# Performance work log

Measured on AMD Instinct MI355X. Metric: run time of the kernel, lower is better.

Reference implementation:

```python
import jax, jax.numpy as jnp
import numpy as np

B, R, A, S, F, N = 2, 1, 16, 14, 1024, 512  # batch, num_rx, num_rx_ant, ofdm_symbols, fft_size, num_effective_sc
D = S * N  # flattened time-frequency dim that C acts on


def setup_inputs() -> dict:
    key = jax.random.key(0)
    k0, k1, k2, k3 = jax.random.split(key, 4)
    scale = 1.0 / np.sqrt(D).astype(np.float32)
    x_re = jax.random.normal(k0, (B, R, A, S, F), jnp.float32)
    x_im = jax.random.normal(k1, (B, R, A, S, F), jnp.float32)
    C_re = jax.random.normal(k2, (D, D), jnp.float32) * scale
    C_im = jax.random.normal(k3, (D, D), jnp.float32) * scale
    # unique, sorted effective-subcarrier indices (as in an OFDM ResourceGrid)
    sc_ind = jnp.asarray(np.sort(np.random.default_rng(0).choice(F, N, replace=False)), jnp.int32)
    return {"x_re": x_re, "x_im": x_im, "C_re": C_re, "C_im": C_im, "sc_ind": sc_ind}


def reference(x_re, x_im, C_re, C_im, sc_ind):
    x = jax.lax.complex(x_re, x_im)            # [B,R,A,S,F] complex64
    C = jax.lax.complex(C_re, C_im)            # [D,D]
    y = jnp.take(x, sc_ind, axis=-1)           # gather effective subcarriers -> [B,R,A,S,N]
    b, r, a, s, n = y.shape
    yf = y.reshape(b, r, a, s * n)             # flatten_last_dims(y, 2)
    # multiply_from_right with adjoint: yf @ C^H
    yf = jnp.einsum('brad,ed->brae', yf, jnp.conj(C))
    y = yf.reshape(b, r, a, s, n)
    # scatter back into full fft_size grid (unique indices -> set == scatter_nd on zeros)
    out = jnp.zeros((b, r, a, s, F), y.dtype).at[..., sc_ind].set(y)
    return jnp.stack([out.real, out.imag])     # [2,B,R,A,S,F] (real, imag)
```

## Files before the change

kernel.cpp:

```cpp
#include <hip/hip_runtime.h>
#include <hip/hip_bf16.h>

#define B_ 2
#define R_ 1
#define A_ 16
#define S_ 14
#define F_ 1024
#define N_ 512
#define D_ (S_*N_)
#define M_ (B_*R_*A_)
#define KK_ (2*D_)
#define BE 64
#define ETILES (D_/BE)

typedef __attribute__((ext_vector_type(8))) short bf16x8;
typedef __attribute__((ext_vector_type(4))) float f32x4;

static __device__ inline short f2bf(float f) {
    __hip_bfloat16 h = __float2bfloat16(f);
    return *reinterpret_cast<short*>(&h);
}
static __device__ inline float bf2f(short s) {
    unsigned int u = ((unsigned int)(unsigned short)s) << 16;
    return __uint_as_float(u);
}

#define LDSP(p) ((__attribute__((address_space(3))) void*)(p))
#define GLBP(p) ((const __attribute__((address_space(1))) void*)(p))

__global__ void prep_kernel(const float* __restrict__ xr, const float* __restrict__ xi,
                            const int* __restrict__ sc, short* __restrict__ Ap) {
    int idx = blockIdx.x * blockDim.x + threadIdx.x;
    if (idx >= 64 * KK_) return;
    int k = idx % KK_;
    int r = idx / KK_;
    int m = r & 31;
    int half = (k >= D_) ? 1 : 0;
    int d = half ? (k - D_) : k;
    int s = d >> 9;
    int n = d & 511;
    int f = sc[n];
    const float* base = (r < 32) ? (half ? xi : xr) : (half ? xr : xi);
    float v = base[(m * S_ + s) * F_ + f];
    if (r >= 32 && half) v = -v;
    Ap[((size_t)(k >> 3) * 64 + r) * 8 + (k & 7)] = f2bf(v);
}

__global__ void zero_kernel(float4* __restrict__ out, int n4) {
    int i = blockIdx.x * blockDim.x + threadIdx.x;
    if (i < n4) out[i] = make_float4(0.f, 0.f, 0.f, 0.f);
}

template<int KSPLIT, int PARTIALS>
__global__ __launch_bounds__(256) void gemm_kernel(
    const short* __restrict__ Ap,
    const float* __restrict__ Cre, const float* __restrict__ Cim,
    const int* __restrict__ sc,
    void* __restrict__ outp)
{
    constexpr int KBLK = KK_ / KSPLIT;
    constexpr int NCH  = KBLK / 32;
    __shared__ float Bl[3][64 * 32];
    __shared__ short Al[3][64 * 32];

    const int etile = blockIdx.x;
    const int ks    = blockIdx.y;
    const int tid   = threadIdx.x;
    const int wave  = tid >> 6;
    const int lane  = tid & 63;
    const int l16   = lane & 15;
    const int kg    = lane >> 4;

    const float* Cp = (ks < KSPLIT / 2) ? Cre : Cim;
    const int kc = (ks % (KSPLIT / 2)) * KBLK;
    const int ka = ks * KBLK;

    const float* bsrc[2];
    #pragma unroll
    for (int q = 0; q < 2; ++q) {
        int U = q * 256 + tid;
        int row = U >> 3;
        int u = (U & 7) ^ (row & 7);
        bsrc[q] = Cp + (size_t)(etile * BE + row) * D_ + kc + u * 4;
    }
    const short* asrc = Ap + ((size_t)(ka >> 3) * 64) * 8 + tid * 8;

#define STAGE(c) do { \
        int bf_ = (c) % 3; \
        __builtin_amdgcn_global_load_lds(GLBP(bsrc[0] + (size_t)(c) * 32), \
                                         LDSP(&Bl[bf_][(0 * 256 + tid) * 4]), 16, 0, 0); \
        __builtin_amdgcn_global_load_lds(GLBP(bsrc[1] + (size_t)(c) * 32), \
                                         LDSP(&Bl[bf_][(1 * 256 + tid) * 4]), 16, 0, 0); \
        __builtin_amdgcn_global_load_lds(GLBP(asrc + (size_t)(c) * 2048), \
                                         LDSP(&Al[bf_][tid * 8]), 16, 0, 0); \
    } while (0)

    STAGE(0);
    STAGE(1);

    f32x4 acc0 = {0.f,0.f,0.f,0.f}, acc1 = {0.f,0.f,0.f,0.f};
    f32x4 acc2 = {0.f,0.f,0.f,0.f}, acc3 = {0.f,0.f,0.f,0.f};

    const int row  = wave * 16 + l16;
    const int swz  = row & 7;
    const int boff = row * 32;
    const int u0 = ((kg * 2 + 0) ^ swz) * 4;
    const int u1 = ((kg * 2 + 1) ^ swz) * 4;

    for (int c = 0; c < NCH; ++c) {
        if (c < NCH - 1) asm volatile("s_waitcnt vmcnt(3)" ::: "memory");
        else             asm volatile("s_waitcnt vmcnt(0)" ::: "memory");
        __builtin_amdgcn_sched_barrier(0);
        __builtin_amdgcn_s_barrier();

        const int buf = c % 3;
        f32x4 b0 = *reinterpret_cast<const f32x4*>(&Bl[buf][boff + u0]);
        f32x4 b1 = *reinterpret_cast<const f32x4*>(&Bl[buf][boff + u1]);
        bf16x8 a0 = *reinterpret_cast<const bf16x8*>(&Al[buf][(kg * 64 + 0 * 16 + l16) * 8]);
        bf16x8 a1 = *reinterpret_cast<const bf16x8*>(&Al[buf][(kg * 64 + 1 * 16 + l16) * 8]);
        bf16x8 a2 = *reinterpret_cast<const bf16x8*>(&Al[buf][(kg * 64 + 2 * 16 + l16) * 8]);
        bf16x8 a3 = *reinterpret_cast<const bf16x8*>(&Al[buf][(kg * 64 + 3 * 16 + l16) * 8]);
        asm volatile("s_waitcnt lgkmcnt(0)" ::: "memory");
        __builtin_amdgcn_sched_barrier(0);
        __builtin_amdgcn_s_barrier();

        if (c + 2 < NCH) STAGE(c + 2);

        bf16x8 bfv;
        bfv[0] = f2bf(b0.x); bfv[1] = f2bf(b0.y); bfv[2] = f2bf(b0.z); bfv[3] = f2bf(b0.w);
        bfv[4] = f2bf(b1.x); bfv[5] = f2bf(b1.y); bfv[6] = f2bf(b1.z); bfv[7] = f2bf(b1.w);
        acc0 = __builtin_amdgcn_mfma_f32_16x16x32_bf16(a0, bfv, acc0, 0, 0, 0);
        acc1 = __builtin_amdgcn_mfma_f32_16x16x32_bf16(a1, bfv, acc1, 0, 0, 0);
        acc2 = __builtin_amdgcn_mfma_f32_16x16x32_bf16(a2, bfv, acc2, 0, 0, 0);
        acc3 = __builtin_amdgcn_mfma_f32_16x16x32_bf16(a3, bfv, acc3, 0, 0, 0);
    }
#undef STAGE

    const int e_lane = etile * BE + row;
    if (PARTIALS) {
        short* part = (short*)outp + (size_t)ks * (64 * D_);
        #pragma unroll
        for (int mt = 0; mt < 4; ++mt) {
            f32x4 a = (mt == 0) ? acc0 : (mt == 1) ? acc1 : (mt == 2) ? acc2 : acc3;
            int rbase = mt * 16 + kg * 4;
            #pragma unroll
            for (int r = 0; r < 4; ++r)
                part[(size_t)(rbase + r) * D_ + e_lane] = f2bf(a[r]);
        }
    } else {
        float* out = (float*)outp;
        int s = e_lane >> 9, n = e_lane & 511;
        int f = sc[n];
        #pragma unroll
        for (int mt = 0; mt < 4; ++mt) {
            f32x4 a = (mt == 0) ? acc0 : (mt == 1) ? acc1 : (mt == 2) ? acc2 : acc3;
            int rbase = mt * 16 + kg * 4;
            #pragma unroll
            for (int r = 0; r < 4; ++r) {
                int rr = rbase + r;
                int pp = rr >> 5, m = rr & 31;
                atomicAdd(&out[((pp * M_ + m) * S_ + s) * F_ + f], a[r]);
            }
        }
    }
}

template<int KSPLIT>
__global__ void reduce_kernel(const short* __restrict__ part, const int* __restrict__ sc,
                              float* __restrict__ out) {
    int t = blockIdx.x * blockDim.x + threadIdx.x;
    if (t >= 64 * D_ / 8) return;
    int base = t * 8;
    int e0 = base % D_;
    int r  = base / D_;
    float v[8] = {0.f,0.f,0.f,0.f,0.f,0.f,0.f,0.f};
    #pragma unroll
    for (int ksp = 0; ksp < KSPLIT; ++ksp) {
        bf16x8 x = *reinterpret_cast<const bf16x8*>(&part[(size_t)ksp * (64 * D_) + base]);
        #pragma unroll
        for (int j = 0; j < 8; ++j) v[j] += bf2f(x[j]);
    }
    int pp = r >> 5, m = r & 31, s = e0 >> 9, n0 = e0 & 511;
    float* ob = &out[((pp * M_ + m) * S_ + s) * F_];
    #pragma unroll
    for (int j = 0; j < 8; ++j) ob[sc[n0 + j]] = v[j];
}

extern "C" void kernel_launch(void* const* d_in, const int* in_sizes, int n_in,
                              void* d_out, int out_size, void* d_ws, size_t ws_size,
                              hipStream_t stream) {
    const float* xr  = (const float*)d_in[0];
    const float* xi  = (const float*)d_in[1];
    const float* Cre = (const float*)d_in[2];
    const float* Cim = (const float*)d_in[3];
    const int*   sc  = (const int*)d_in[4];
    float* out = (float*)d_out;

    short* Ap = (short*)d_ws;
    const size_t partOff = 2u * 1024u * 1024u;
    const size_t need28  = partOff + 28ull * 64 * D_ * 2;
    const size_t need16  = partOff + 16ull * 64 * D_ * 2;

    prep_kernel<<<dim3((64 * KK_ + 255) / 256), 256, 0, stream>>>(xr, xi, sc, Ap);
    zero_kernel<<<dim3((917504 / 4 + 255) / 256), 256, 0, stream>>>((float4*)out, 917504 / 4);

    const int rthreads = 64 * D_ / 8;
    if (ws_size >= need28) {
        short* part = (short*)((char*)d_ws + partOff);
        gemm_kernel<28, 1><<<dim3(ETILES, 28), 256, 0, stream>>>(Ap, Cre, Cim, sc, part);
        reduce_kernel<28><<<dim3((rthreads + 255) / 256), 256, 0, stream>>>(part, sc, out);
    } else if (ws_size >= need16) {
        short* part = (short*)((char*)d_ws + partOff);
        gemm_kernel<16, 1><<<dim3(ETILES, 16), 256, 0, stream>>>(Ap, Cre, Cim, sc, part);
        reduce_kernel<16><<<dim3((rthreads + 255) / 256), 256, 0, stream>>>(part, sc, out);
    } else {
        gemm_kernel<16, 0><<<dim3(ETILES, 16), 256, 0, stream>>>(Ap, Cre, Cim, sc, out);
    }
}
```

Measured before the change: 107.7 us.

## Make each wave load its own tiles and drop block barriers in split-K GEMM

```diff
diff --git a/kernel.cpp b/kernel.cpp
--- a/kernel.cpp
+++ b/kernel.cpp
@@ -51,8 +51,109 @@
     if (i < n4) out[i] = make_float4(0.f, 0.f, 0.f, 0.f);
 }
 
+__global__ __launch_bounds__(256) void gemm_wasync(
+    const short* __restrict__ Ap,
+    const float* __restrict__ Cre, const float* __restrict__ Cim,
+    short* __restrict__ part_all)
+{
+    constexpr int KSPLIT = 28;
+    constexpr int KBLK = KK_ / KSPLIT;
+    constexpr int NCH  = KBLK / 32;
+    __shared__ float Bl[4][3][16 * 32];
+    __shared__ short Al[4][3][64 * 32];
+
+    const int etile = blockIdx.x;
+    const int ks    = blockIdx.y;
+    const int tid   = threadIdx.x;
+    const int wave  = tid >> 6;
+    const int lane  = tid & 63;
+    const int l16   = lane & 15;
+    const int kg    = lane >> 4;
+
+    const float* Cp = (ks < 14) ? Cre : Cim;
+    const int kc = (ks % 14) * KBLK;
+    const int ka = ks * KBLK;
+
+    const int U0 = lane, U1 = 64 + lane;
+    const float* bsrc0 = Cp + (size_t)(etile * 64 + wave * 16 + (U0 >> 3)) * D_
+                            + kc + ((U0 & 7) ^ ((U0 >> 3) & 7)) * 4;
+    const float* bsrc1 = Cp + (size_t)(etile * 64 + wave * 16 + (U1 >> 3)) * D_
+                            + kc + ((U1 & 7) ^ ((U1 >> 3) & 7)) * 4;
+    const short* asrc = Ap + (size_t)(ka >> 3) * 512 + lane * 8;
+
+#define WAITV(n) asm volatile("s_waitcnt vmcnt(" #n ")" ::: "memory")
+#define STAGE(cc) do { \
+        int bb = (cc) % 3; \
+        __builtin_amdgcn_global_load_lds(GLBP(bsrc0 + (size_t)(cc) * 32), \
+                                         LDSP(&Bl[wave][bb][lane * 4]), 16, 0, 0); \
+        __builtin_amdgcn_global_load_lds(GLBP(bsrc1 + (size_t)(cc) * 32), \
+                                         LDSP(&Bl[wave][bb][(64 + lane) * 4]), 16, 0, 0); \
+        __builtin_amdgcn_global_load_lds(GLBP(asrc + (size_t)(cc) * 2048 + 0 * 512), \
+                                         LDSP(&Al[wave][bb][lane * 8]), 16, 0, 0); \
+        __builtin_amdgcn_global_load_lds(GLBP(asrc + (size_t)(cc) * 2048 + 1 * 512), \
+                                         LDSP(&Al[wave][bb][(64 + lane) * 8]), 16, 0, 0); \
+        __builtin_amdgcn_global_load_lds(GLBP(asrc + (size_t)(cc) * 2048 + 2 * 512), \
+                                         LDSP(&Al[wave][bb][(128 + lane) * 8]), 16, 0, 0); \
+        __builtin_amdgcn_global_load_lds(GLBP(asrc + (size_t)(cc) * 2048 + 3 * 512), \
+                                         LDSP(&Al[wave][bb][(192 + lane) * 8]), 16, 0, 0); \
+    } while (0)
+
+    STAGE(0);
+    STAGE(1);
+    STAGE(2);
+
+    f32x4 acc0 = {0.f,0.f,0.f,0.f}, acc1 = {0.f,0.f,0.f,0.f};
+    f32x4 acc2 = {0.f,0.f,0.f,0.f}, acc3 = {0.f,0.f,0.f,0.f};
+
+    const int swz  = l16 & 7;
+    const int boff = l16 * 32;
+    const int u0x = ((kg * 2 + 0) ^ swz) * 4;
+    const int u1x = ((kg * 2 + 1) ^ swz) * 4;
+
+    for (int c = 0; c < NCH; ++c) {
+        if (c <= NCH - 3)      { WAITV(12); }
+        else if (c == NCH - 2) { WAITV(6); }
+        else                   { WAITV(0); }
+        __builtin_amdgcn_sched_barrier(0);
+
+        const int buf = c % 3;
+        f32x4 b0 = *reinterpret_cast<const f32x4*>(&Bl[wave][buf][boff + u0x]);
+        f32x4 b1 = *reinterpret_cast<const f32x4*>(&Bl[wave][buf][boff + u1x]);
+        bf16x8 a0 = *reinterpret_cast<const bf16x8*>(&Al[wave][buf][(kg * 64 + 0 * 16 + l16) * 8]);
+        bf16x8 a1 = *reinterpret_cast<const bf16x8*>(&Al[wave][buf][(kg * 64 + 1 * 16 + l16) * 8]);
+        bf16x8 a2 = *reinterpret_cast<const bf16x8*>(&Al[wave][buf][(kg * 64 + 2 * 16 + l16) * 8]);
+        bf16x8 a3 = *reinterpret_cast<const bf16x8*>(&Al[wave][buf][(kg * 64 + 3 * 16 + l16) * 8]);
+        asm volatile("s_waitcnt lgkmcnt(0)" ::: "memory");
+        __builtin_amdgcn_sched_barrier(0);
+
+        if (c + 3 < NCH) STAGE(c + 3);
+        __builtin_amdgcn_sched_barrier(0);
+
+        bf16x8 bfv;
+        bfv[0] = f2bf(b0.x); bfv[1] = f2bf(b0.y); bfv[2] = f2bf(b0.z); bfv[3] = f2bf(b0.w);
+        bfv[4] = f2bf(b1.x); bfv[5] = f2bf(b1.y); bfv[6] = f2bf(b1.z); bfv[7] = f2bf(b1.w);
+        acc0 = __builtin_amdgcn_mfma_f32_16x16x32_bf16(a0, bfv, acc0, 0, 0, 0);
+        acc1 = __builtin_amdgcn_mfma_f32_16x16x32_bf16(a1, bfv, acc1, 0, 0, 0);
+        acc2 = __builtin_amdgcn_mfma_f32_16x16x32_bf16(a2, bfv, acc2, 0, 0, 0);
+        acc3 = __builtin_amdgcn_mfma_f32_16x16x32_bf16(a3, bfv, acc3, 0, 0, 0);
+    }
+#undef STAGE
+#undef WAITV
+
+    const int e_lane = etile * 64 + wave * 16 + l16;
+    short* part = part_all + (size_t)ks * (64 * D_);
+    #pragma unroll
+    for (int mt = 0; mt < 4; ++mt) {
+        f32x4 a = (mt == 0) ? acc0 : (mt == 1) ? acc1 : (mt == 2) ? acc2 : acc3;
+        int rbase = mt * 16 + kg * 4;
+        #pragma unroll
+        for (int r = 0; r < 4; ++r)
+            part[(size_t)(rbase + r) * D_ + e_lane] = f2bf(a[r]);
+    }
+}
+
 template<int KSPLIT, int PARTIALS>
-__global__ __launch_bounds__(256) void gemm_kernel(
+__global__ __launch_bounds__(256) void gemm_sync(
     const short* __restrict__ Ap,
     const float* __restrict__ Cre, const float* __restrict__ Cim,
     const int* __restrict__ sc,
@@ -60,8 +161,8 @@
 {
     constexpr int KBLK = KK_ / KSPLIT;
     constexpr int NCH  = KBLK / 32;
-    __shared__ float Bl[3][64 * 32];
-    __shared__ short Al[3][64 * 32];
+    __shared__ float Bls[3][64 * 32];
+    __shared__ short Als[3][64 * 32];
 
     const int etile = blockIdx.x;
     const int ks    = blockIdx.y;
@@ -85,18 +186,18 @@
     }
     const short* asrc = Ap + ((size_t)(ka >> 3) * 64) * 8 + tid * 8;
 
-#define STAGE(c) do { \
+#define STG(c) do { \
         int bf_ = (c) % 3; \
         __builtin_amdgcn_global_load_lds(GLBP(bsrc[0] + (size_t)(c) * 32), \
-                                         LDSP(&Bl[bf_][(0 * 256 + tid) * 4]), 16, 0, 0); \
+                                         LDSP(&Bls[bf_][(0 * 256 + tid) * 4]), 16, 0, 0); \
         __builtin_amdgcn_global_load_lds(GLBP(bsrc[1] + (size_t)(c) * 32), \
-                                         LDSP(&Bl[bf_][(1 * 256 + tid) * 4]), 16, 0, 0); \
+                                         LDSP(&Bls[bf_][(1 * 256 + tid) * 4]), 16, 0, 0); \
         __builtin_amdgcn_global_load_lds(GLBP(asrc + (size_t)(c) * 2048), \
-                                         LDSP(&Al[bf_][tid * 8]), 16, 0, 0); \
+                                         LDSP(&Als[bf_][tid * 8]), 16, 0, 0); \
     } while (0)
 
-    STAGE(0);
-    STAGE(1);
+    STG(0);
+    STG(1);
 
     f32x4 acc0 = {0.f,0.f,0.f,0.f}, acc1 = {0.f,0.f,0.f,0.f};
     f32x4 acc2 = {0.f,0.f,0.f,0.f}, acc3 = {0.f,0.f,0.f,0.f};
@@ -114,17 +215,17 @@
         __builtin_amdgcn_s_barrier();
 
         const int buf = c % 3;
-        f32x4 b0 = *reinterpret_cast<const f32x4*>(&Bl[buf][boff + u0]);
-        f32x4 b1 = *reinterpret_cast<const f32x4*>(&Bl[buf][boff + u1]);
-        bf16x8 a0 = *reinterpret_cast<const bf16x8*>(&Al[buf][(kg * 64 + 0 * 16 + l16) * 8]);
-        bf16x8 a1 = *reinterpret_cast<const bf16x8*>(&Al[buf][(kg * 64 + 1 * 16 + l16) * 8]);
-        bf16x8 a2 = *reinterpret_cast<const bf16x8*>(&Al[buf][(kg * 64 + 2 * 16 + l16) * 8]);
-        bf16x8 a3 = *reinterpret_cast<const bf16x8*>(&Al[buf][(kg * 64 + 3 * 16 + l16) * 8]);
+        f32x4 b0 = *reinterpret_cast<const f32x4*>(&Bls[buf][boff + u0]);
+        f32x4 b1 = *reinterpret_cast<const f32x4*>(&Bls[buf][boff + u1]);
+        bf16x8 a0 = *reinterpret_cast<const bf16x8*>(&Als[buf][(kg * 64 + 0 * 16 + l16) * 8]);
+        bf16x8 a1 = *reinterpret_cast<const bf16x8*>(&Als[buf][(kg * 64 + 1 * 16 + l16) * 8]);
+        bf16x8 a2 = *reinterpret_cast<const bf16x8*>(&Als[buf][(kg * 64 + 2 * 16 + l16) * 8]);
+        bf16x8 a3 = *reinterpret_cast<const bf16x8*>(&Als[buf][(kg * 64 + 3 * 16 + l16) * 8]);
         asm volatile("s_waitcnt lgkmcnt(0)" ::: "memory");
         __builtin_amdgcn_sched_barrier(0);
         __builtin_amdgcn_s_barrier();
 
-        if (c + 2 < NCH) STAGE(c + 2);
+        if (c + 2 < NCH) STG(c + 2);
 
         bf16x8 bfv;
         bfv[0] = f2bf(b0.x); bfv[1] = f2bf(b0.y); bfv[2] = f2bf(b0.z); bfv[3] = f2bf(b0.w);
@@ -134,7 +235,7 @@
         acc2 = __builtin_amdgcn_mfma_f32_16x16x32_bf16(a2, bfv, acc2, 0, 0, 0);
         acc3 = __builtin_amdgcn_mfma_f32_16x16x32_bf16(a3, bfv, acc3, 0, 0, 0);
     }
-#undef STAGE
+#undef STG
 
     const int e_lane = etile * BE + row;
     if (PARTIALS) {
@@ -207,13 +308,13 @@
     const int rthreads = 64 * D_ / 8;
     if (ws_size >= need28) {
         short* part = (short*)((char*)d_ws + partOff);
-        gemm_kernel<28, 1><<<dim3(ETILES, 28), 256, 0, stream>>>(Ap, Cre, Cim, sc, part);
+        gemm_wasync<<<dim3(ETILES, 28), 256, 0, stream>>>(Ap, Cre, Cim, part);
         reduce_kernel<28><<<dim3((rthreads + 255) / 256), 256, 0, stream>>>(part, sc, out);
     } else if (ws_size >= need16) {
         short* part = (short*)((char*)d_ws + partOff);
-        gemm_kernel<16, 1><<<dim3(ETILES, 16), 256, 0, stream>>>(Ap, Cre, Cim, sc, part);
+        gemm_sync<16, 1><<<dim3(ETILES, 16), 256, 0, stream>>>(Ap, Cre, Cim, sc, part);
         reduce_kernel<16><<<dim3((rthreads + 255) / 256), 256, 0, stream>>>(part, sc, out);
     } else {
-        gemm_kernel<16, 0><<<dim3(ETILES, 16), 256, 0, stream>>>(Ap, Cre, Cim, sc, out);
-    }
-}
+        gemm_sync<16, 0><<<dim3(ETILES, 16), 256, 0, stream>>>(Ap, Cre, Cim, sc, out);
+    }
+}
```

Result: slower. 123.8 us (+15.0%).
